# Kernel optimization log

Hardware: AMD Instinct MI355X
Metric: run time of the kernel (lower is better)

The kernel has to match this reference:

```python
import jax, jax.numpy as jnp
import numpy as np

N = 100000       # nodes
E = 3200000      # edges (avg degree 32)
IN_F = 256
OUT_F = 128


def setup_inputs() -> dict:
    key = jax.random.key(0)
    k1, k2, k3, k4, k5, k6 = jax.random.split(key, 6)
    x = jax.random.normal(k1, (N, IN_F), dtype=jnp.float32)
    adj_row = jax.random.randint(k2, (E,), 0, N, dtype=jnp.int64)
    adj_col = jax.random.randint(k3, (E,), 0, N, dtype=jnp.int64)
    adj_val = jax.random.uniform(k4, (E,), dtype=jnp.float32)
    stdv = 1.0 / np.sqrt(OUT_F)
    weight = jax.random.uniform(k5, (IN_F, OUT_F), dtype=jnp.float32, minval=-stdv, maxval=stdv)
    bias = jax.random.uniform(k6, (OUT_F,), dtype=jnp.float32, minval=-stdv, maxval=stdv)
    return {"x": x, "adj_row": adj_row, "adj_col": adj_col,
            "adj_val": adj_val, "weight": weight, "bias": bias}


def reference(x, adj_row, adj_col, adj_val, weight, bias):
    # dropout with p=0 is identity
    support = x @ weight                                   # [N, OUT_F] dense GEMM
    # spmm(adj, support): gather neighbor rows, scale by edge value, segment-sum into rows
    gathered = adj_val[:, None] * support[adj_col]         # [E, OUT_F]
    out = jax.ops.segment_sum(gathered, adj_row, num_segments=N)  # [N, OUT_F]
    return jax.nn.relu(out + bias)
```

## Files before the change

kernel.cpp:

```cpp
#include <hip/hip_runtime.h>

#define N_NODES 100000
#define IN_F 256
#define OUT_F 128
#define RPB 64
#define RSHIFT 6
#define NB 1563
#define CAPG 2432
#define CHUNK_SC 4096

typedef short bf16x8 __attribute__((ext_vector_type(8)));
typedef float f32x4  __attribute__((ext_vector_type(4)));

static __device__ __forceinline__ unsigned short f2bf(float f) {
    unsigned int u = __float_as_uint(f);
    u = (u + 0x7FFF + ((u >> 16) & 1)) >> 16;
    return (unsigned short)u;
}

__global__ __launch_bounds__(256) void wt_kernel(const float* __restrict__ w,
                                                 unsigned short* __restrict__ wT,
                                                 int* __restrict__ gcur) {
    int n = blockIdx.x;
    int k = threadIdx.x;
    wT[n * IN_F + k] = f2bf(w[(size_t)k * OUT_F + n]);
    if (blockIdx.x < 7) {
        int i = blockIdx.x * 256 + threadIdx.x;
        if (i < NB) gcur[i] = i * CAPG;
    }
}

__global__ __launch_bounds__(256) void gemm_mfma_kernel(const float* __restrict__ x,
                                                        const unsigned short* __restrict__ wT,
                                                        unsigned short* __restrict__ supb) {
    __shared__ unsigned short A_lds[32][264];

    const int tid  = threadIdx.x;
    const int wave = tid >> 6;
    const int lane = tid & 63;
    const int quad = lane >> 4;
    const int l15  = lane & 15;
    const int row_base = blockIdx.x * 32;

    bf16x8 bfrag[2][8];
    {
        const unsigned short* wb = wT + (size_t)(wave * 32 + l15) * IN_F + quad * 8;
#pragma unroll
        for (int ct = 0; ct < 2; ++ct)
#pragma unroll
            for (int ks = 0; ks < 8; ++ks)
                bfrag[ct][ks] = *(const bf16x8*)(wb + ct * 16 * IN_F + ks * 32);
    }

    {
        const float* xb = x + (size_t)row_base * IN_F;
#pragma unroll
        for (int i = 0; i < 8; ++i) {
            int fidx = i * 1024 + tid * 4;
            float4 a = *(const float4*)(xb + fidx);
            int r = fidx >> 8;
            int c = fidx & 255;
            ushort4 u = {f2bf(a.x), f2bf(a.y), f2bf(a.z), f2bf(a.w)};
            *(ushort4*)&A_lds[r][c] = u;
        }
    }
    __syncthreads();

    f32x4 acc[2][2];
#pragma unroll
    for (int rt = 0; rt < 2; ++rt)
#pragma unroll
        for (int ct = 0; ct < 2; ++ct) acc[rt][ct] = (f32x4){0.f, 0.f, 0.f, 0.f};

#pragma unroll
    for (int ks = 0; ks < 8; ++ks) {
        bf16x8 a0 = *(const bf16x8*)&A_lds[l15][ks * 32 + quad * 8];
        bf16x8 a1 = *(const bf16x8*)&A_lds[16 + l15][ks * 32 + quad * 8];
        acc[0][0] = __builtin_amdgcn_mfma_f32_16x16x32_bf16(a0, bfrag[0][ks], acc[0][0], 0, 0, 0);
        acc[0][1] = __builtin_amdgcn_mfma_f32_16x16x32_bf16(a0, bfrag[1][ks], acc[0][1], 0, 0, 0);
        acc[1][0] = __builtin_amdgcn_mfma_f32_16x16x32_bf16(a1, bfrag[0][ks], acc[1][0], 0, 0, 0);
        acc[1][1] = __builtin_amdgcn_mfma_f32_16x16x32_bf16(a1, bfrag[1][ks], acc[1][1], 0, 0, 0);
    }

#pragma unroll
    for (int rt = 0; rt < 2; ++rt)
#pragma unroll
        for (int ct = 0; ct < 2; ++ct)
#pragma unroll
            for (int r = 0; r < 4; ++r) {
                int orow = row_base + rt * 16 + quad * 4 + r;
                int ocol = wave * 32 + ct * 16 + l15;
                supb[(size_t)orow * OUT_F + ocol] = f2bf(acc[rt][ct][r]);
            }
}

__global__ __launch_bounds__(512) void scatter_kernel(const int* __restrict__ adj_row,
                                                      const int* __restrict__ adj_col,
                                                      const float* __restrict__ adj_val,
                                                      int* __restrict__ gcur,
                                                      int2* __restrict__ ebuf, int E) {
    __shared__ int pref[NB + 1];
    __shared__ int shf[NB];
    __shared__ int2 se[CHUNK_SC];
    __shared__ short sbk[CHUNK_SC];
    __shared__ int wsum[8];

    const int tid  = threadIdx.x;
    const int base = blockIdx.x * CHUNK_SC;
    const int m    = min(CHUNK_SC, E - base);
    const int nv   = m >> 2;

    for (int b = tid; b <= NB; b += 512) pref[b] = 0;
    __syncthreads();

    for (int j = tid; j < nv; j += 512) {
        int4 r4 = ((const int4*)(adj_row + base))[j];
        atomicAdd(&pref[r4.x >> RSHIFT], 1);
        atomicAdd(&pref[r4.y >> RSHIFT], 1);
        atomicAdd(&pref[r4.z >> RSHIFT], 1);
        atomicAdd(&pref[r4.w >> RSHIFT], 1);
    }
    if (tid < (m & 3)) atomicAdd(&pref[adj_row[base + (nv << 2) + tid] >> RSHIFT], 1);
    __syncthreads();

    {
        int loc[4];
        const int bb = tid * 4;
        int s = 0;
#pragma unroll
        for (int g = 0; g < 4; ++g) {
            int b = bb + g;
            int v = (b < NB) ? pref[b] : 0;
            loc[g] = s;
            s += v;
        }
        const int lane = tid & 63, wv = tid >> 6;
        int inc = s;
        for (int d = 1; d < 64; d <<= 1) {
            int t = __shfl_up(inc, d, 64);
            if (lane >= d) inc += t;
        }
        if (lane == 63) wsum[wv] = inc;
        __syncthreads();
        int wb2 = 0;
        for (int k = 0; k < wv; ++k) wb2 += wsum[k];
        const int texcl = wb2 + inc - s;
#pragma unroll
        for (int g = 0; g < 4; ++g) {
            int b = bb + g;
            if (b < NB) pref[b] = texcl + loc[g];
        }
        if (tid == 511) pref[NB] = texcl + s;
    }
    __syncthreads();

    for (int b = tid; b < NB; b += 512) {
        int s0 = pref[b];
        int c  = pref[b + 1] - s0;
        if (c > 0) shf[b] = atomicAdd(&gcur[b], c) - s0;
    }
    __syncthreads();

    for (int j = tid; j < nv; j += 512) {
        int4   c4 = ((const int4*)(adj_col + base))[j];
        int4   r4 = ((const int4*)(adj_row + base))[j];
        float4 v4 = ((const float4*)(adj_val + base))[j];
        int p, bk;
        bk = r4.x >> RSHIFT; p = atomicAdd(&pref[bk], 1);
        se[p] = make_int2(c4.x | ((r4.x & (RPB - 1)) << 17), __float_as_int(v4.x)); sbk[p] = (short)bk;
        bk = r4.y >> RSHIFT; p = atomicAdd(&pref[bk], 1);
        se[p] = make_int2(c4.y | ((r4.y & (RPB - 1)) << 17), __float_as_int(v4.y)); sbk[p] = (short)bk;
        bk = r4.z >> RSHIFT; p = atomicAdd(&pref[bk], 1);
        se[p] = make_int2(c4.z | ((r4.z & (RPB - 1)) << 17), __float_as_int(v4.z)); sbk[p] = (short)bk;
        bk = r4.w >> RSHIFT; p = atomicAdd(&pref[bk], 1);
        se[p] = make_int2(c4.w | ((r4.w & (RPB - 1)) << 17), __float_as_int(v4.w)); sbk[p] = (short)bk;
    }
    if (tid < (m & 3)) {
        int i = base + (nv << 2) + tid;
        int r = adj_row[i];
        int bk = r >> RSHIFT;
        int p = atomicAdd(&pref[bk], 1);
        se[p] = make_int2(adj_col[i] | ((r & (RPB - 1)) << 17), __float_as_int(adj_val[i]));
        sbk[p] = (short)bk;
    }
    __syncthreads();

    for (int p = tid; p < m; p += 512) {
        int bk = sbk[p];
        int g = shf[bk] + p;
        if (g < (bk + 1) * CAPG) ebuf[g] = se[p];
    }
}

__global__ __launch_bounds__(256) void spmm_kernel(const int2* __restrict__ ebuf,
                                                   const int* __restrict__ gcur,
                                                   const unsigned short* __restrict__ supb,
                                                   const float* __restrict__ bias,
                                                   float* __restrict__ out) {
    __shared__ int2 se[CAPG];
    __shared__ int cnt[RPB];
    __shared__ int off[RPB];
    __shared__ int cur[RPB];

    const int tid  = threadIdx.x;
    const int b    = blockIdx.x;
    const int wave = tid >> 6;
    const int lane = tid & 63;
    const int f0   = lane * 2;

    const int start = b * CAPG;
    int m = gcur[b] - start;
    if (m > CAPG) m = CAPG;

    if (tid < RPB) cnt[tid] = 0;
    __syncthreads();

    int2 ev[10];
#pragma unroll
    for (int j = 0; j < 10; ++j) {
        int i = j * 256 + tid;
        if (i < m) {
            ev[j] = ebuf[start + i];
            atomicAdd(&cnt[ev[j].x >> 17], 1);
        }
    }
    __syncthreads();

    if (tid < RPB) {
        int v = cnt[tid];
        int s = v;
#pragma unroll
        for (int d = 1; d < RPB; d <<= 1) {
            int t = __shfl_up(s, d, 64);
            if (tid >= d) s += t;
        }
        off[tid] = s - v;
        cur[tid] = s - v;
    }
    __syncthreads();

#pragma unroll
    for (int j = 0; j < 10; ++j) {
        int i = j * 256 + tid;
        if (i < m) {
            int p = atomicAdd(&cur[ev[j].x >> 17], 1);
            se[p] = ev[j];
        }
    }
    __syncthreads();

    float2 acc[16];
#pragma unroll
    for (int j = 0; j < 16; ++j) acc[j] = make_float2(0.f, 0.f);

#pragma unroll
    for (int j = 0; j < 16; ++j) {
        int r = wave * 16 + j;
        int o = off[r];
        int c = cnt[r];
        float2 a = acc[j];
        int i = 0;
        for (; i + 4 <= c; i += 4) {
            int2 e0 = se[o + i + 0];
            int2 e1 = se[o + i + 1];
            int2 e2 = se[o + i + 2];
            int2 e3 = se[o + i + 3];
            unsigned int u0 = *(const unsigned int*)(supb + (size_t)(e0.x & 0x1FFFF) * OUT_F + f0);
            unsigned int u1 = *(const unsigned int*)(supb + (size_t)(e1.x & 0x1FFFF) * OUT_F + f0);
            unsigned int u2 = *(const unsigned int*)(supb + (size_t)(e2.x & 0x1FFFF) * OUT_F + f0);
            unsigned int u3 = *(const unsigned int*)(supb + (size_t)(e3.x & 0x1FFFF) * OUT_F + f0);
            float v0 = __int_as_float(e0.y), v1 = __int_as_float(e1.y);
            float v2 = __int_as_float(e2.y), v3 = __int_as_float(e3.y);
            a.x += v0 * __uint_as_float(u0 << 16);
            a.y += v0 * __uint_as_float(u0 & 0xFFFF0000u);
            a.x += v1 * __uint_as_float(u1 << 16);
            a.y += v1 * __uint_as_float(u1 & 0xFFFF0000u);
            a.x += v2 * __uint_as_float(u2 << 16);
            a.y += v2 * __uint_as_float(u2 & 0xFFFF0000u);
            a.x += v3 * __uint_as_float(u3 << 16);
            a.y += v3 * __uint_as_float(u3 & 0xFFFF0000u);
        }
        for (; i < c; ++i) {
            int2 e = se[o + i];
            unsigned int u = *(const unsigned int*)(supb + (size_t)(e.x & 0x1FFFF) * OUT_F + f0);
            float v = __int_as_float(e.y);
            a.x += v * __uint_as_float(u << 16);
            a.y += v * __uint_as_float(u & 0xFFFF0000u);
        }
        acc[j] = a;
    }

    float2 bv = *((const float2*)bias + lane);
    const int rbase = b << RSHIFT;
#pragma unroll
    for (int j = 0; j < 16; ++j) {
        int grow = rbase + wave * 16 + j;
        if (grow < N_NODES) {
            float2 o;
            o.x = fmaxf(acc[j].x + bv.x, 0.f);
            o.y = fmaxf(acc[j].y + bv.y, 0.f);
            *((float2*)(out + (size_t)grow * OUT_F) + lane) = o;
        }
    }
}

extern "C" void kernel_launch(void* const* d_in, const int* in_sizes, int n_in,
                              void* d_out, int out_size, void* d_ws, size_t ws_size,
                              hipStream_t stream) {
    const float* x       = (const float*)d_in[0];
    const int*   adj_row = (const int*)d_in[1];
    const int*   adj_col = (const int*)d_in[2];
    const float* adj_val = (const float*)d_in[3];
    const float* weight  = (const float*)d_in[4];
    const float* bias    = (const float*)d_in[5];
    float* out = (float*)d_out;
    const int E = in_sizes[1];

    char* p = (char*)d_ws;
    unsigned short* supb = (unsigned short*)p;  p += (size_t)N_NODES * OUT_F * 2;
    int2* ebuf           = (int2*)p;            p += (size_t)NB * CAPG * 8;
    unsigned short* wT   = (unsigned short*)p;  p += (size_t)OUT_F * IN_F * 2;
    int* gcur            = (int*)p;             p += (size_t)NB * 4;

    wt_kernel<<<OUT_F, 256, 0, stream>>>(weight, wT, gcur);
    gemm_mfma_kernel<<<N_NODES / 32, 256, 0, stream>>>(x, wT, supb);
    scatter_kernel<<<(E + CHUNK_SC - 1) / CHUNK_SC, 512, 0, stream>>>(adj_row, adj_col,
                                                                      adj_val, gcur, ebuf, E);
    spmm_kernel<<<NB, 256, 0, stream>>>(ebuf, gcur, supb, bias, out);
}
```

Before: 364.3 us.

## Sort edges by column slice within each row block for gather locality

```diff
diff --git a/kernel.cpp b/kernel.cpp
--- a/kernel.cpp
+++ b/kernel.cpp
@@ -8,6 +8,8 @@
 #define NB 1563
 #define CAPG 2432
 #define CHUNK_SC 4096
+#define NSLC 8
+#define NKEY (NSLC * RPB)
 
 typedef short bf16x8 __attribute__((ext_vector_type(8)));
 typedef float f32x4  __attribute__((ext_vector_type(4)));
@@ -198,9 +200,9 @@
                                                    const float* __restrict__ bias,
                                                    float* __restrict__ out) {
     __shared__ int2 se[CAPG];
-    __shared__ int cnt[RPB];
-    __shared__ int off[RPB];
-    __shared__ int cur[RPB];
+    __shared__ int off[NKEY];
+    __shared__ int cur[NKEY];
+    __shared__ int wsum[4];
 
     const int tid  = threadIdx.x;
     const int b    = blockIdx.x;
@@ -212,30 +214,42 @@
     int m = gcur[b] - start;
     if (m > CAPG) m = CAPG;
 
-    if (tid < RPB) cnt[tid] = 0;
+    cur[tid] = 0;
+    cur[tid + 256] = 0;
     __syncthreads();
 
     int2 ev[10];
+    int kk[10];
 #pragma unroll
     for (int j = 0; j < 10; ++j) {
         int i = j * 256 + tid;
         if (i < m) {
             ev[j] = ebuf[start + i];
-            atomicAdd(&cnt[ev[j].x >> 17], 1);
-        }
-    }
-    __syncthreads();
-
-    if (tid < RPB) {
-        int v = cnt[tid];
-        int s = v;
-#pragma unroll
-        for (int d = 1; d < RPB; d <<= 1) {
-            int t = __shfl_up(s, d, 64);
-            if (tid >= d) s += t;
-        }
-        off[tid] = s - v;
-        cur[tid] = s - v;
+            int x = ev[j].x;
+            kk[j] = (((x >> 14) & 7) << 6) | (x >> 17);
+            atomicAdd(&cur[kk[j]], 1);
+        }
+    }
+    __syncthreads();
+
+    {
+        const int k0 = tid * 2;
+        int v0 = cur[k0], v1 = cur[k0 + 1];
+        int s = v0 + v1;
+        const int ln = tid & 63, wv = tid >> 6;
+        int inc = s;
+#pragma unroll
+        for (int d = 1; d < 64; d <<= 1) {
+            int t = __shfl_up(inc, d, 64);
+            if (ln >= d) inc += t;
+        }
+        if (ln == 63) wsum[wv] = inc;
+        __syncthreads();
+        int wb = 0;
+        for (int k = 0; k < wv; ++k) wb += wsum[k];
+        int excl = wb + inc - s;
+        off[k0]     = excl;      cur[k0]     = excl;
+        off[k0 + 1] = excl + v0; cur[k0 + 1] = excl + v0;
     }
     __syncthreads();
 
@@ -243,7 +257,7 @@
     for (int j = 0; j < 10; ++j) {
         int i = j * 256 + tid;
         if (i < m) {
-            int p = atomicAdd(&cur[ev[j].x >> 17], 1);
+            int p = atomicAdd(&cur[kk[j]], 1);
             se[p] = ev[j];
         }
     }
@@ -253,41 +267,42 @@
 #pragma unroll
     for (int j = 0; j < 16; ++j) acc[j] = make_float2(0.f, 0.f);
 
-#pragma unroll
-    for (int j = 0; j < 16; ++j) {
-        int r = wave * 16 + j;
-        int o = off[r];
-        int c = cnt[r];
-        float2 a = acc[j];
-        int i = 0;
-        for (; i + 4 <= c; i += 4) {
-            int2 e0 = se[o + i + 0];
-            int2 e1 = se[o + i + 1];
-            int2 e2 = se[o + i + 2];
-            int2 e3 = se[o + i + 3];
-            unsigned int u0 = *(const unsigned int*)(supb + (size_t)(e0.x & 0x1FFFF) * OUT_F + f0);
-            unsigned int u1 = *(const unsigned int*)(supb + (size_t)(e1.x & 0x1FFFF) * OUT_F + f0);
-            unsigned int u2 = *(const unsigned int*)(supb + (size_t)(e2.x & 0x1FFFF) * OUT_F + f0);
-            unsigned int u3 = *(const unsigned int*)(supb + (size_t)(e3.x & 0x1FFFF) * OUT_F + f0);
-            float v0 = __int_as_float(e0.y), v1 = __int_as_float(e1.y);
-            float v2 = __int_as_float(e2.y), v3 = __int_as_float(e3.y);
-            a.x += v0 * __uint_as_float(u0 << 16);
-            a.y += v0 * __uint_as_float(u0 & 0xFFFF0000u);
-            a.x += v1 * __uint_as_float(u1 << 16);
-            a.y += v1 * __uint_as_float(u1 & 0xFFFF0000u);
-            a.x += v2 * __uint_as_float(u2 << 16);
-            a.y += v2 * __uint_as_float(u2 & 0xFFFF0000u);
-            a.x += v3 * __uint_as_float(u3 << 16);
-            a.y += v3 * __uint_as_float(u3 & 0xFFFF0000u);
-        }
-        for (; i < c; ++i) {
-            int2 e = se[o + i];
-            unsigned int u = *(const unsigned int*)(supb + (size_t)(e.x & 0x1FFFF) * OUT_F + f0);
-            float v = __int_as_float(e.y);
-            a.x += v * __uint_as_float(u << 16);
-            a.y += v * __uint_as_float(u & 0xFFFF0000u);
-        }
-        acc[j] = a;
+    for (int slc = 0; slc < 7; ++slc) {
+#pragma unroll
+        for (int j = 0; j < 16; ++j) {
+            const int k = (slc << 6) | (wave * 16 + j);
+            int i = off[k];
+            const int e = cur[k];
+            float2 a = acc[j];
+            for (; i + 4 <= e; i += 4) {
+                int2 e0 = se[i + 0];
+                int2 e1 = se[i + 1];
+                int2 e2 = se[i + 2];
+                int2 e3 = se[i + 3];
+                unsigned int u0 = *(const unsigned int*)(supb + (size_t)(e0.x & 0x1FFFF) * OUT_F + f0);
+                unsigned int u1 = *(const unsigned int*)(supb + (size_t)(e1.x & 0x1FFFF) * OUT_F + f0);
+                unsigned int u2 = *(const unsigned int*)(supb + (size_t)(e2.x & 0x1FFFF) * OUT_F + f0);
+                unsigned int u3 = *(const unsigned int*)(supb + (size_t)(e3.x & 0x1FFFF) * OUT_F + f0);
+                float v0 = __int_as_float(e0.y), v1 = __int_as_float(e1.y);
+                float v2 = __int_as_float(e2.y), v3 = __int_as_float(e3.y);
+                a.x += v0 * __uint_as_float(u0 << 16);
+                a.y += v0 * __uint_as_float(u0 & 0xFFFF0000u);
+                a.x += v1 * __uint_as_float(u1 << 16);
+                a.y += v1 * __uint_as_float(u1 & 0xFFFF0000u);
+                a.x += v2 * __uint_as_float(u2 << 16);
+                a.y += v2 * __uint_as_float(u2 & 0xFFFF0000u);
+                a.x += v3 * __uint_as_float(u3 << 16);
+                a.y += v3 * __uint_as_float(u3 & 0xFFFF0000u);
+            }
+            for (; i < e; ++i) {
+                int2 ee = se[i];
+                unsigned int u = *(const unsigned int*)(supb + (size_t)(ee.x & 0x1FFFF) * OUT_F + f0);
+                float v = __int_as_float(ee.y);
+                a.x += v * __uint_as_float(u << 16);
+                a.y += v * __uint_as_float(u & 0xFFFF0000u);
+            }
+            acc[j] = a;
+        }
     }
 
     float2 bv = *((const float2*)bias + lane);
```

After: 442.8 us. 21.5% more time.
